# Kernel tuning notes

Measured on AMD Instinct MI355X. Metric: run time of the kernel, lower is better.

Reference implementation:

```python
import jax, jax.numpy as jnp
import numpy as np

NFRAMES = 8
N_ITERS = 32        # fixed-iteration Riemannian gradient descent (geomstats FrechetMean equivalent)
EPS = 1e-7


def _l2norm(x, axis=-1):
    return x / jnp.maximum(jnp.linalg.norm(x, axis=axis, keepdims=True), EPS)


def _frechet_mean_sphere(X):
    """Batched Frechet mean on the unit hypersphere.
    X: [..., n, d] unit vectors. Returns [..., d] unit mean.
    Iteration: mu <- Exp_mu( mean_i Log_mu(x_i) ).
    """
    mu0 = _l2norm(jnp.mean(X, axis=-2))

    def step(mu, _):
        dots = jnp.clip(jnp.einsum('...d,...kd->...k', mu, X), -1.0 + 1e-6, 1.0 - 1e-6)
        theta = jnp.arccos(dots)
        safe = theta > 1e-4
        coef = jnp.where(safe, theta / jnp.sin(jnp.where(safe, theta, 1.0)), 1.0)
        # Log map: [..., n, d]
        logs = coef[..., None] * (X - dots[..., None] * mu[..., None, :])
        v = jnp.mean(logs, axis=-2)                      # tangent mean [..., d]
        vn = jnp.linalg.norm(v, axis=-1, keepdims=True)
        vsafe = vn > 1e-9
        sinc = jnp.where(vsafe, jnp.sin(vn) / jnp.where(vsafe, vn, 1.0), 1.0)
        mu_new = jnp.cos(vn) * mu + sinc * v             # Exp map
        return _l2norm(mu_new), None

    mu, _ = jax.lax.scan(step, mu0, None, length=N_ITERS)
    return mu


def setup_inputs() -> dict:
    key = jax.random.key(0)
    k1, k2 = jax.random.split(key)
    support_vecs = jax.random.normal(k1, (25, 64, NFRAMES * 2048), dtype=jnp.float32)
    target_vec = jax.random.normal(k2, (64, NFRAMES * 2048), dtype=jnp.float32)
    return {"support_vecs": support_vecs, "target_vec": target_vec}


def reference(support_vecs, target_vec):
    seqlen, bs, df = support_vecs.shape
    sup = _l2norm(support_vecs.reshape(seqlen, bs, NFRAMES, -1))   # [s,b,n,2048]
    tgt = _l2norm(target_vec.reshape(bs, NFRAMES, -1))             # [b,n,2048]
    support_means = _frechet_mean_sphere(sup)                      # [s,b,2048]
    target_means = _frechet_mean_sphere(tgt)                       # [b,2048]
    similarities = jnp.einsum('sbd,bd->sb', support_means, target_means)
    return similarities
```

## Files before the change

### kernel.cpp

```cpp
#include <hip/hip_runtime.h>
#include <math.h>

#define NFR 8
#define DD 2048
#define NS 25
#define NB 64
#define NPAIR (NS*NB)
#define NITER 32

typedef __attribute__((ext_vector_type(8))) short short8;
typedef __attribute__((ext_vector_type(4))) float f32x4;

__device__ __forceinline__ float acos_fast(float x) {
    const float ax = fabsf(x);
    const bool big = ax > 0.5f;
    const float z = big ? 0.5f * (1.f - ax) : x * x;
    const float s = big ? sqrtf(z) : ax;
    float p = fmaf(z, 4.2163199048e-2f, 2.4181311049e-2f);
    p = fmaf(z, p, 4.5470025998e-2f);
    p = fmaf(z, p, 7.4953002686e-2f);
    p = fmaf(z, p, 1.6666752422e-1f);
    const float asin_s = fmaf(s * z, p, s);
    const float asin_abs = big ? (1.5707963267948966f - 2.f * asin_s) : asin_s;
    return 1.5707963267948966f - copysignf(asin_abs, x);
}

#define SPLIT2(a, b, HI, LO) { \
    const float ha_ = __uint_as_float(__float_as_uint(a) & 0xFFFF0000u); \
    const float hb_ = __uint_as_float(__float_as_uint(b) & 0xFFFF0000u); \
    HI = __builtin_amdgcn_perm(__float_as_uint(b), __float_as_uint(a), 0x07060302u); \
    LO = __builtin_amdgcn_perm(__float_as_uint((b) - hb_), __float_as_uint((a) - ha_), 0x07060302u); \
}

__global__ __launch_bounds__(256) void fused_kernel(const float* __restrict__ sup,
                                                    const float* __restrict__ tgt,
                                                    float* __restrict__ out) {
    const int p   = blockIdx.x;
    const int tid = threadIdx.x;
    const int wv  = tid >> 6;
    const int l   = tid & 63;
    const int row = l & 15;
    const int kg  = l >> 4;

    __shared__ float part[4][16][17];
    __shared__ float graw[256];

    const float* rowp = (row < 8)
        ? sup + (size_t)p * (NFR*DD) + (size_t)row * DD
        : tgt + (size_t)(p & (NB-1)) * (NFR*DD) + (size_t)(row - 8) * DD;
    const float4* lp = (const float4*)rowp + (wv * 128 + kg * 2);

    float4 fA[3], fB[3];
    fA[0] = lp[0];  fB[0] = lp[1];
    fA[1] = lp[8];  fB[1] = lp[9];
    fA[2] = lp[16]; fB[2] = lp[17];

    f32x4 accA = {0.f, 0.f, 0.f, 0.f};
    f32x4 accB = {0.f, 0.f, 0.f, 0.f};
    #pragma unroll
    for (int c = 0; c < 16; ++c) {
        const int s = c % 3;
        const float4 f0 = fA[s];
        const float4 f1 = fB[s];
        if (c + 3 < 16) {
            fA[s] = lp[(c + 3) * 8];
            fB[s] = lp[(c + 3) * 8 + 1];
        }
        union { unsigned int u[4]; short8 s8; } H, L;
        SPLIT2(f0.x, f0.y, H.u[0], L.u[0]);
        SPLIT2(f0.z, f0.w, H.u[1], L.u[1]);
        SPLIT2(f1.x, f1.y, H.u[2], L.u[2]);
        SPLIT2(f1.z, f1.w, H.u[3], L.u[3]);
        accA = __builtin_amdgcn_mfma_f32_16x16x32_bf16(H.s8, H.s8, accA, 0, 0, 0);
        accB = __builtin_amdgcn_mfma_f32_16x16x32_bf16(H.s8, L.s8, accB, 0, 0, 0);
        accB = __builtin_amdgcn_mfma_f32_16x16x32_bf16(L.s8, H.s8, accB, 0, 0, 0);
    }
    #pragma unroll
    for (int r = 0; r < 4; ++r)
        part[wv][kg * 4 + r][row] = accA[r] + accB[r];
    __syncthreads();

    {
        const int rr = tid >> 4, cc = tid & 15;
        graw[rr * 16 + cc] = part[0][rr][cc] + part[1][rr][cc]
                           + part[2][rr][cc] + part[3][rr][cc];
    }
    __syncthreads();

    if (tid < 16) {
        const int j = tid & 7;
        const int base = tid & 8;
        const int R = base + j;
        const int cb = base;

        const float invn_own = rsqrtf(fmaxf(graw[R * 16 + R], 1e-14f));
        float Grow[8];
        #pragma unroll
        for (int k = 0; k < 8; ++k) {
            const float invk = rsqrtf(fmaxf(graw[(cb + k) * 16 + (cb + k)], 1e-14f));
            Grow[k] = graw[R * 16 + cb + k] * invn_own * invk;
        }

        float rs = 0.f;
        #pragma unroll
        for (int k = 0; k < 8; ++k) rs += Grow[k];
        rs += __shfl_xor(rs, 1, 8);
        rs += __shfl_xor(rs, 2, 8);
        rs += __shfl_xor(rs, 4, 8);
        float a_own = rsqrtf(fmaxf(rs, 6.4e-13f));
        float aAll[8];
        #pragma unroll
        for (int k = 0; k < 8; ++k) aAll[k] = a_own;

        for (int it = 0; it < NITER; ++it) {
            float dot = 0.f;
            #pragma unroll
            for (int k = 0; k < 8; ++k) dot = fmaf(Grow[k], aAll[k], dot);
            dot = fminf(fmaxf(dot, -1.f + 1e-6f), 1.f - 1e-6f);
            const float theta = acos_fast(dot);
            const float q = fmaf(-dot, dot, 1.0f);
            const float coef = (theta > 1e-4f) ? theta * rsqrtf(q) : 1.f;
            const float w = 0.125f * coef;
            float wAll[8];
            #pragma unroll
            for (int k = 0; k < 8; ++k) wAll[k] = __shfl(w, base + k, 16);
            float Gw = 0.f;
            #pragma unroll
            for (int k = 0; k < 8; ++k) Gw = fmaf(Grow[k], wAll[k], Gw);
            float u1 = a_own * Gw, u2 = w * Gw;
            u1 += __shfl_xor(u1, 1, 8);  u2 += __shfl_xor(u2, 1, 8);
            u1 += __shfl_xor(u1, 2, 8);  u2 += __shfl_xor(u2, 2, 8);
            u1 += __shfl_xor(u1, 4, 8);  u2 += __shfl_xor(u2, 4, 8);
            const float cdavg = u1;
            const float vnsq = fmaxf(u2 - cdavg * cdavg, 0.f);
            const float vn = sqrtf(vnsq);
            const float rev = vn * 0.15915494309189535f;
            const float sinv = __builtin_amdgcn_sinf(rev);
            const float cosv = __builtin_amdgcn_cosf(rev);
            const float sinc = (vn > 1e-9f) ? sinv / vn : 1.f;
            const float cn2 = fmaf(sinc * sinc, vnsq, cosv * cosv);
            const float rn = rsqrtf(fmaxf(cn2, 1e-14f));
            a_own = (cosv * a_own + sinc * fmaf(-cdavg, a_own, w)) * rn;
            #pragma unroll
            for (int k = 0; k < 8; ++k)
                aAll[k] = (cosv * aAll[k] + sinc * fmaf(-cdavg, aAll[k], wAll[k])) * rn;
        }

        const float ahat = a_own * invn_own;
        float at[8];
        #pragma unroll
        for (int q2 = 0; q2 < 8; ++q2) at[q2] = __shfl(ahat, 8 + q2, 16);
        float tacc = 0.f;
        #pragma unroll
        for (int q2 = 0; q2 < 8; ++q2) tacc = fmaf(graw[j * 16 + 8 + q2], at[q2], tacc);
        float sim = ahat * tacc;
        sim += __shfl_xor(sim, 1, 8);
        sim += __shfl_xor(sim, 2, 8);
        sim += __shfl_xor(sim, 4, 8);
        if (tid == 0) out[p] = sim;
    }
}

extern "C" void kernel_launch(void* const* d_in, const int* in_sizes, int n_in,
                              void* d_out, int out_size, void* d_ws, size_t ws_size,
                              hipStream_t stream) {
    const float* sup = (const float*)d_in[0];
    const float* tgt = (const float*)d_in[1];
    float* out = (float*)d_out;
    fused_kernel<<<NPAIR, 256, 0, stream>>>(sup, tgt, out);
}
```

Before: 51.33 us.

## Stream Gram inputs through double-buffered LDS via direct global-to-LDS loads

Replaces the per-thread register prefetch pipeline with `global_load_lds` DMA transfers that fill a double-buffered LDS tile of 16 rows × 256 floats. The block grows to 512 threads, so 8 waves each compute a k-slice of the Gram matrix, and the partials are reduced over 8 waves instead of 4. The goal is to raise memory-level parallelism and cut VGPR pressure on this bandwidth-bound load phase. The cost is a block-wide barrier per tile, larger LDS use that may limit occupancy, and reliance on the barrier to wait for the asynchronous LDS loads to complete.

```diff
diff --git a/kernel.cpp b/kernel.cpp
--- a/kernel.cpp
+++ b/kernel.cpp
@@ -7,6 +7,11 @@
 #define NB 64
 #define NPAIR (NS*NB)
 #define NITER 32
+#define TPB 512
+#define CHUNK 256
+#define NTILE (DD/CHUNK)
+#define ROWF (CHUNK+4)
+#define BUFF (16*ROWF)
 
 typedef __attribute__((ext_vector_type(8))) short short8;
 typedef __attribute__((ext_vector_type(4))) float f32x4;
@@ -32,7 +37,13 @@
     LO = __builtin_amdgcn_perm(__float_as_uint((b) - hb_), __float_as_uint((a) - ha_), 0x07060302u); \
 }
 
-__global__ __launch_bounds__(256) void fused_kernel(const float* __restrict__ sup,
+__device__ __forceinline__ void load_lds16(const float* g, float* l) {
+    __builtin_amdgcn_global_load_lds(
+        (const __attribute__((address_space(1))) void*)g,
+        (__attribute__((address_space(3))) void*)l, 16, 0, 0);
+}
+
+__global__ __launch_bounds__(TPB) void fused_kernel(const float* __restrict__ sup,
                                                     const float* __restrict__ tgt,
                                                     float* __restrict__ out) {
     const int p   = blockIdx.x;
@@ -42,30 +53,35 @@
     const int row = l & 15;
     const int kg  = l >> 4;
 
-    __shared__ float part[4][16][17];
-    __shared__ float graw[256];
+    __shared__ float lds[2 * BUFF];
+    float* part = lds;
+    float* graw = lds + 2176;
 
-    const float* rowp = (row < 8)
-        ? sup + (size_t)p * (NFR*DD) + (size_t)row * DD
-        : tgt + (size_t)(p & (NB-1)) * (NFR*DD) + (size_t)(row - 8) * DD;
-    const float4* lp = (const float4*)rowp + (wv * 128 + kg * 2);
-
-    float4 fA[3], fB[3];
-    fA[0] = lp[0];  fB[0] = lp[1];
-    fA[1] = lp[8];  fB[1] = lp[9];
-    fA[2] = lp[16]; fB[2] = lp[17];
+    const int r0 = 2 * wv;
+    const float* gA = (wv < 4)
+        ? sup + ((size_t)p * NFR + r0) * DD + l * 4
+        : tgt + ((size_t)(p & (NB-1)) * NFR + (r0 - 8)) * DD + l * 4;
+    const float* gB = gA + DD;
+    float* dA0 = lds + r0 * ROWF;            float* dA1 = dA0 + BUFF;
+    float* dB0 = lds + (r0 + 1) * ROWF;      float* dB1 = dB0 + BUFF;
+    const float* frag0 = lds + row * ROWF + wv * 32 + kg * 8;
+    const float* frag1 = frag0 + BUFF;
 
     f32x4 accA = {0.f, 0.f, 0.f, 0.f};
     f32x4 accB = {0.f, 0.f, 0.f, 0.f};
+
+    load_lds16(gA, dA0);
+    load_lds16(gB, dB0);
+    __syncthreads();
     #pragma unroll
-    for (int c = 0; c < 16; ++c) {
-        const int s = c % 3;
-        const float4 f0 = fA[s];
-        const float4 f1 = fB[s];
-        if (c + 3 < 16) {
-            fA[s] = lp[(c + 3) * 8];
-            fB[s] = lp[(c + 3) * 8 + 1];
+    for (int t = 0; t < NTILE; ++t) {
+        if (t + 1 < NTILE) {
+            if (((t + 1) & 1) == 0) { load_lds16(gA + (t+1)*CHUNK, dA0); load_lds16(gB + (t+1)*CHUNK, dB0); }
+            else                    { load_lds16(gA + (t+1)*CHUNK, dA1); load_lds16(gB + (t+1)*CHUNK, dB1); }
         }
+        const float* fb = ((t & 1) == 0) ? frag0 : frag1;
+        const float4 f0 = *(const float4*)fb;
+        const float4 f1 = *(const float4*)(fb + 4);
         union { unsigned int u[4]; short8 s8; } H, L;
         SPLIT2(f0.x, f0.y, H.u[0], L.u[0]);
         SPLIT2(f0.z, f0.w, H.u[1], L.u[1]);
@@ -74,16 +90,20 @@
         accA = __builtin_amdgcn_mfma_f32_16x16x32_bf16(H.s8, H.s8, accA, 0, 0, 0);
         accB = __builtin_amdgcn_mfma_f32_16x16x32_bf16(H.s8, L.s8, accB, 0, 0, 0);
         accB = __builtin_amdgcn_mfma_f32_16x16x32_bf16(L.s8, H.s8, accB, 0, 0, 0);
+        __syncthreads();
     }
+
     #pragma unroll
     for (int r = 0; r < 4; ++r)
-        part[wv][kg * 4 + r][row] = accA[r] + accB[r];
+        part[wv * 272 + (kg * 4 + r) * 17 + row] = accA[r] + accB[r];
     __syncthreads();
 
-    {
+    if (tid < 256) {
         const int rr = tid >> 4, cc = tid & 15;
-        graw[rr * 16 + cc] = part[0][rr][cc] + part[1][rr][cc]
-                           + part[2][rr][cc] + part[3][rr][cc];
+        float s = 0.f;
+        #pragma unroll
+        for (int w = 0; w < 8; ++w) s += part[w * 272 + rr * 17 + cc];
+        graw[rr * 16 + cc] = s;
     }
     __syncthreads();
 
@@ -167,5 +187,5 @@
     const float* sup = (const float*)d_in[0];
     const float* tgt = (const float*)d_in[1];
     float* out = (float*)d_out;
-    fused_kernel<<<NPAIR, 256, 0, stream>>>(sup, tgt, out);
+    fused_kernel<<<NPAIR, TPB, 0, stream>>>(sup, tgt, out);
 }
```

Result: slower. 61.26 us (+19.3%).

## Process two support sequences per block to share target loads

Applied to the files above, without the earlier changes.

Each block now handles two support indices for one batch element. It loads the target rows once and computes three 8x8 Gram blocks (sup-sup, sup-tgt, tgt-tgt) with split-bf16 MFMAs, then runs two Frechet iterations in parallel on 32 lanes. This roughly halves the redundant target-vector reads, since the old kernel reread them for all 25 support indices, and it halves the block count. In exchange each block issues 9 MFMAs per chunk instead of 3. The last group recomputes a duplicate support row whose result is discarded.

```diff
diff --git a/kernel.cpp b/kernel.cpp
--- a/kernel.cpp
+++ b/kernel.cpp
@@ -5,7 +5,10 @@
 #define DD 2048
 #define NS 25
 #define NB 64
-#define NPAIR (NS*NB)
+#define NSG 13
+#define NBLK (NB*NSG)
+#define TPB 256
+#define NCH 16
 #define NITER 32
 
 typedef __attribute__((ext_vector_type(8))) short short8;
@@ -32,64 +35,105 @@
     LO = __builtin_amdgcn_perm(__float_as_uint((b) - hb_), __float_as_uint((a) - ha_), 0x07060302u); \
 }
 
-__global__ __launch_bounds__(256) void fused_kernel(const float* __restrict__ sup,
+__global__ __launch_bounds__(TPB) void fused_kernel(const float* __restrict__ sup,
                                                     const float* __restrict__ tgt,
                                                     float* __restrict__ out) {
-    const int p   = blockIdx.x;
+    const int b   = blockIdx.x / NSG;
+    const int sg  = blockIdx.x % NSG;
     const int tid = threadIdx.x;
     const int wv  = tid >> 6;
     const int l   = tid & 63;
     const int row = l & 15;
     const int kg  = l >> 4;
 
-    __shared__ float part[4][16][17];
-    __shared__ float graw[256];
-
-    const float* rowp = (row < 8)
-        ? sup + (size_t)p * (NFR*DD) + (size_t)row * DD
-        : tgt + (size_t)(p & (NB-1)) * (NFR*DD) + (size_t)(row - 8) * DD;
-    const float4* lp = (const float4*)rowp + (wv * 128 + kg * 2);
-
-    float4 fA[3], fB[3];
-    fA[0] = lp[0];  fB[0] = lp[1];
-    fA[1] = lp[8];  fB[1] = lp[9];
-    fA[2] = lp[16]; fB[2] = lp[17];
-
-    f32x4 accA = {0.f, 0.f, 0.f, 0.f};
-    f32x4 accB = {0.f, 0.f, 0.f, 0.f};
+    __shared__ float part[4 * 768];
+    __shared__ float gsum[768];
+    __shared__ float synth[512];
+
+    const int s0 = 2 * sg;
+    const int s1 = (2 * sg + 1 < NS) ? 2 * sg + 1 : NS - 1;
+    const int srow = (row < 8) ? s0 : s1;
+    const float* aptr = sup + (((size_t)srow * NB + b) * NFR + (row & 7)) * DD + wv * 512 + kg * 8;
+    const float* tptr = tgt + ((size_t)b * NFR + (row & 7)) * DD + wv * 512 + kg * 8;
+
+    f32x4 acc11 = {0.f,0.f,0.f,0.f}, acc12 = {0.f,0.f,0.f,0.f};
+    f32x4 acc21 = {0.f,0.f,0.f,0.f}, acc22 = {0.f,0.f,0.f,0.f};
+    f32x4 acc31 = {0.f,0.f,0.f,0.f}, acc32 = {0.f,0.f,0.f,0.f};
+
+    float4 pa0[2], pa1[2], pt0[2], pt1[2];
+    pa0[0] = *(const float4*)(aptr +  0); pa1[0] = *(const float4*)(aptr +  4);
+    pt0[0] = *(const float4*)(tptr +  0); pt1[0] = *(const float4*)(tptr +  4);
+    pa0[1] = *(const float4*)(aptr + 32); pa1[1] = *(const float4*)(aptr + 36);
+    pt0[1] = *(const float4*)(tptr + 32); pt1[1] = *(const float4*)(tptr + 36);
+
     #pragma unroll
-    for (int c = 0; c < 16; ++c) {
-        const int s = c % 3;
-        const float4 f0 = fA[s];
-        const float4 f1 = fB[s];
-        if (c + 3 < 16) {
-            fA[s] = lp[(c + 3) * 8];
-            fB[s] = lp[(c + 3) * 8 + 1];
-        }
-        union { unsigned int u[4]; short8 s8; } H, L;
-        SPLIT2(f0.x, f0.y, H.u[0], L.u[0]);
-        SPLIT2(f0.z, f0.w, H.u[1], L.u[1]);
-        SPLIT2(f1.x, f1.y, H.u[2], L.u[2]);
-        SPLIT2(f1.z, f1.w, H.u[3], L.u[3]);
-        accA = __builtin_amdgcn_mfma_f32_16x16x32_bf16(H.s8, H.s8, accA, 0, 0, 0);
-        accB = __builtin_amdgcn_mfma_f32_16x16x32_bf16(H.s8, L.s8, accB, 0, 0, 0);
-        accB = __builtin_amdgcn_mfma_f32_16x16x32_bf16(L.s8, H.s8, accB, 0, 0, 0);
-    }
-    #pragma unroll
-    for (int r = 0; r < 4; ++r)
-        part[wv][kg * 4 + r][row] = accA[r] + accB[r];
+    for (int c = 0; c < NCH; ++c) {
+        const int sl = c & 1;
+        const float4 fa0 = pa0[sl], fa1 = pa1[sl];
+        const float4 ft0 = pt0[sl], ft1 = pt1[sl];
+        if (c + 2 < NCH) {
+            pa0[sl] = *(const float4*)(aptr + (c+2)*32);
+            pa1[sl] = *(const float4*)(aptr + (c+2)*32 + 4);
+            pt0[sl] = *(const float4*)(tptr + (c+2)*32);
+            pt1[sl] = *(const float4*)(tptr + (c+2)*32 + 4);
+        }
+        union { unsigned int u[4]; short8 s8; } AH, AL, TH, TL;
+        SPLIT2(fa0.x, fa0.y, AH.u[0], AL.u[0]);
+        SPLIT2(fa0.z, fa0.w, AH.u[1], AL.u[1]);
+        SPLIT2(fa1.x, fa1.y, AH.u[2], AL.u[2]);
+        SPLIT2(fa1.z, fa1.w, AH.u[3], AL.u[3]);
+        SPLIT2(ft0.x, ft0.y, TH.u[0], TL.u[0]);
+        SPLIT2(ft0.z, ft0.w, TH.u[1], TL.u[1]);
+        SPLIT2(ft1.x, ft1.y, TH.u[2], TL.u[2]);
+        SPLIT2(ft1.z, ft1.w, TH.u[3], TL.u[3]);
+        acc11 = __builtin_amdgcn_mfma_f32_16x16x32_bf16(AH.s8, AH.s8, acc11, 0, 0, 0);
+        acc12 = __builtin_amdgcn_mfma_f32_16x16x32_bf16(AH.s8, AL.s8, acc12, 0, 0, 0);
+        acc12 = __builtin_amdgcn_mfma_f32_16x16x32_bf16(AL.s8, AH.s8, acc12, 0, 0, 0);
+        acc21 = __builtin_amdgcn_mfma_f32_16x16x32_bf16(AH.s8, TH.s8, acc21, 0, 0, 0);
+        acc22 = __builtin_amdgcn_mfma_f32_16x16x32_bf16(AH.s8, TL.s8, acc22, 0, 0, 0);
+        acc22 = __builtin_amdgcn_mfma_f32_16x16x32_bf16(AL.s8, TH.s8, acc22, 0, 0, 0);
+        acc31 = __builtin_amdgcn_mfma_f32_16x16x32_bf16(TH.s8, TH.s8, acc31, 0, 0, 0);
+        acc32 = __builtin_amdgcn_mfma_f32_16x16x32_bf16(TH.s8, TL.s8, acc32, 0, 0, 0);
+        acc32 = __builtin_amdgcn_mfma_f32_16x16x32_bf16(TL.s8, TH.s8, acc32, 0, 0, 0);
+    }
+
+    {
+        float* mp = part + wv * 768;
+        #pragma unroll
+        for (int r = 0; r < 4; ++r) {
+            const int idx = (kg * 4 + r) * 16 + row;
+            mp[      idx] = acc11[r] + acc12[r];
+            mp[256 + idx] = acc21[r] + acc22[r];
+            mp[512 + idx] = acc31[r] + acc32[r];
+        }
+    }
     __syncthreads();
 
-    {
-        const int rr = tid >> 4, cc = tid & 15;
-        graw[rr * 16 + cc] = part[0][rr][cc] + part[1][rr][cc]
-                           + part[2][rr][cc] + part[3][rr][cc];
+    for (int i = tid; i < 768; i += TPB) {
+        float s = part[i] + part[768 + i] + part[1536 + i] + part[2304 + i];
+        gsum[i] = s;
     }
     __syncthreads();
 
-    if (tid < 16) {
-        const int j = tid & 7;
-        const int base = tid & 8;
+    for (int e2 = tid; e2 < 512; e2 += TPB) {
+        const int g = e2 >> 8, e = e2 & 255;
+        const int i = e >> 4, j = e & 15;
+        float v = 0.f;
+        if (i < 8)
+            v = (j < 8) ? gsum[(i + 8*g) * 16 + (j + 8*g)]
+                        : gsum[256 + (i + 8*g) * 16 + (j - 8)];
+        else if (j >= 8)
+            v = gsum[512 + (i - 8) * 16 + (j - 8)];
+        synth[e2] = v;
+    }
+    __syncthreads();
+
+    if (tid < 32) {
+        const int g = tid >> 4;
+        const int t16 = tid & 15;
+        const float* graw = synth + g * 256;
+        const int j = t16 & 7;
+        const int base = t16 & 8;
         const int R = base + j;
         const int cb = base;
 
@@ -157,7 +201,10 @@
         sim += __shfl_xor(sim, 1, 8);
         sim += __shfl_xor(sim, 2, 8);
         sim += __shfl_xor(sim, 4, 8);
-        if (tid == 0) out[p] = sim;
+        if (t16 == 0) {
+            const int s = 2 * sg + g;
+            if (s < NS) out[s * NB + b] = sim;
+        }
     }
 }
 
@@ -167,5 +214,5 @@
     const float* sup = (const float*)d_in[0];
     const float* tgt = (const float*)d_in[1];
     float* out = (float*)d_out;
-    fused_kernel<<<NPAIR, 256, 0, stream>>>(sup, tgt, out);
-}
+    fused_kernel<<<NBLK, TPB, 0, stream>>>(sup, tgt, out);
+}
```

Result: no change. 52.07 us (+1.4%).
